# Performance work log

Measured on AMD Instinct MI355X. Metric: run time of the kernel, lower is better.

## Reference

```python
import jax, jax.numpy as jnp
import numpy as np

L, H, P, R = 4096, 1024, 512, 16
DT_MIN, DT_MAX = 1e-3, 1e-1

def setup_inputs() -> dict:
    key = jax.random.key(0)
    ks = jax.random.split(key, 16)
    return {
        "input_sequence": jax.random.normal(ks[0], (L, H), jnp.float32),
        # HiPPO-like eigenvalues: negative real part, spread imaginary part
        "Lambda_re": (-0.5 * jax.random.uniform(ks[1], (P,), jnp.float32) - 1e-2),
        "Lambda_im": 3.0 * jax.random.normal(ks[2], (P,), jnp.float32),
        "B_re": jax.random.normal(ks[3], (P, H), jnp.float32) / np.float32(np.sqrt(H)),
        "B_im": jax.random.normal(ks[4], (P, H), jnp.float32) / np.float32(np.sqrt(H)),
        "C_re": jax.random.normal(ks[5], (H, 2 * P), jnp.float32) / np.float32(np.sqrt(2 * P)),
        "C_im": jax.random.normal(ks[6], (H, 2 * P), jnp.float32) / np.float32(np.sqrt(2 * P)),
        "E_re": 0.01 * jax.random.normal(ks[7], (P, R), jnp.float32),
        "E_im": 0.01 * jax.random.normal(ks[8], (P, R), jnp.float32),
        "F_re": 0.01 * jax.random.normal(ks[9], (R, P), jnp.float32),
        "F_im": 0.01 * jax.random.normal(ks[10], (R, P), jnp.float32),
        "D": jax.random.normal(ks[11], (H,), jnp.float32),
        "log_step": np.float32(np.log(DT_MIN)) + jax.random.uniform(ks[12], (P,), jnp.float32) * np.float32(np.log(DT_MAX) - np.log(DT_MIN)),
        "Delta_t_diag": 0.01 * jax.random.normal(ks[13], (L, R), jnp.float32),
    }

def _scan_op(q_i, q_j):
    # diagonal linear recurrence combine: x_j = A_j * x_i + b_j
    A_i, b_i = q_i
    A_j, b_j = q_j
    return (A_j * A_i, A_j * b_i + b_j)

def reference(input_sequence, Lambda_re, Lambda_im, B_re, B_im, C_re, C_im,
              E_re, E_im, F_re, F_im, D, log_step, Delta_t_diag):
    # clip_eigs=True: enforce left-half-plane
    Lam = jnp.clip(Lambda_re, None, -1e-4) + 1j * Lambda_im            # (P,)
    step = jnp.exp(log_step)                                           # (P,)  step_rescale=1.0
    # zoh discretization
    Lambda_bar = jnp.exp(Lam * step)                                   # (P,)
    B_tilde = B_re + 1j * B_im                                         # (P,H)
    B_bar = ((Lambda_bar - 1.0) / Lam)[:, None] * B_tilde              # (P,H)
    # Lambda extension: diag(E @ diag(d_l) @ F)[p] = sum_r E[p,r] d_l[r] F[r,p]
    E = E_re + 1j * E_im                                               # (P,R)
    F = F_re + 1j * F_im                                               # (R,P)
    EF = E.T * F                                                       # (R,P)
    ext = Delta_t_diag.astype(EF.dtype) @ EF                           # (L,P)
    Lambda_elements = Lambda_bar[None, :] + ext                        # (L,P)
    Bu_elements = input_sequence.astype(B_bar.dtype) @ B_bar.T         # (L,P)
    _, xs_f = jax.lax.associative_scan(_scan_op, (Lambda_elements, Bu_elements))
    _, xs_b = jax.lax.associative_scan(_scan_op, (Lambda_elements, Bu_elements), reverse=True)
    xs = jnp.concatenate((xs_f, xs_b), axis=-1)                        # (L,2P) bidirectional
    C_tilde = C_re + 1j * C_im                                         # (H,2P)
    ys = 2.0 * (xs @ C_tilde.T).real                                   # conj_sym=True -> 2*Re
    return ys + D * input_sequence                                     # feedthrough
```

## Files before the change

### kernel.cpp

```cpp
#include <hip/hip_runtime.h>

#define LL 4096
#define HH 1024
#define PP 512
#define RR 16
#define CH 128
#define CL 32

typedef _Float16 f16x8 __attribute__((ext_vector_type(8)));
typedef float f32x4 __attribute__((ext_vector_type(4)));
typedef unsigned short u16;
typedef unsigned int u32;

#define MF16(a, b, c) __builtin_amdgcn_mfma_f32_16x16x32_f16(a, b, c, 0, 0, 0)

__device__ __forceinline__ u16 h16(float x) {
  _Float16 h = (_Float16)x;
  return __builtin_bit_cast(u16, h);
}
__device__ __forceinline__ float f16f(u16 v) {
  return (float)__builtin_bit_cast(_Float16, v);
}

__global__ void precompute_kernel(const float* __restrict__ Lre, const float* __restrict__ Lim,
                                  const float* __restrict__ lst,
                                  const float* __restrict__ Ere, const float* __restrict__ Eim,
                                  const float* __restrict__ Fre, const float* __restrict__ Fim,
                                  float* __restrict__ Lbr, float* __restrict__ Lbi,
                                  float* __restrict__ cfr, float* __restrict__ cfi,
                                  float* __restrict__ EFr, float* __restrict__ EFi)
{
  int p = blockIdx.x * blockDim.x + threadIdx.x;
  if (p >= PP) return;
  float lre = fminf(Lre[p], -1e-4f);
  float lim = Lim[p];
  float st  = expf(lst[p]);
  float er  = expf(lre * st);
  float s, c;
  sincosf(lim * st, &s, &c);
  float lbr = er * c, lbi = er * s;
  Lbr[p] = lbr; Lbi[p] = lbi;
  float den = lre * lre + lim * lim;
  float nr  = lbr - 1.0f;
  cfr[p] = (nr * lre + lbi * lim) / den;
  cfi[p] = (lbi * lre - nr * lim) / den;
  for (int r = 0; r < RR; ++r) {
    float e_r = Ere[p * RR + r], e_i = Eim[p * RR + r];
    float f_r = Fre[r * PP + p], f_i = Fim[r * PP + p];
    EFr[r * PP + p] = e_r * f_r - e_i * f_i;
    EFi[r * PP + p] = e_r * f_i + e_i * f_r;
  }
}

__global__ __launch_bounds__(256) void prep2_kernel(
    const float* __restrict__ Bre, const float* __restrict__ Bim,
    const float* __restrict__ cfr, const float* __restrict__ cfi,
    const float* __restrict__ Cre, const float* __restrict__ Cim,
    const float* __restrict__ Dt, const float* __restrict__ EFr,
    const float* __restrict__ EFi,
    u16* __restrict__ B1, u32* __restrict__ B2, u32* __restrict__ LE)
{
  int g = blockIdx.x, t = threadIdx.x;
  if (g < 512) {
    int base = (g * 256 + t) * 4;
    int p = base >> 10, col = base & 1023;
    float cr = cfr[p], ci = cfi[p];
    float4 br = *(const float4*)&Bre[base];
    float4 bi = *(const float4*)&Bim[base];
    ushort4 rp, ip;
    rp.x = h16(cr*br.x - ci*bi.x); ip.x = h16(cr*bi.x + ci*br.x);
    rp.y = h16(cr*br.y - ci*bi.y); ip.y = h16(cr*bi.y + ci*br.y);
    rp.z = h16(cr*br.z - ci*bi.z); ip.z = h16(cr*bi.z + ci*br.z);
    rp.w = h16(cr*br.w - ci*bi.w); ip.w = h16(cr*bi.w + ci*br.w);
    *(ushort4*)&B1[(size_t)(2 * p) * 1024 + col] = rp;
    *(ushort4*)&B1[(size_t)(2 * p + 1) * 1024 + col] = ip;
  } else if (g < 1536) {
    int base = ((g - 512) * 256 + t) * 4;
    float4 a = *(const float4*)&Cre[base];
    float4 b = *(const float4*)&Cim[base];
    uint4 o;
    o.x = (u32)h16(a.x) | ((u32)h16(-b.x) << 16);
    o.y = (u32)h16(a.y) | ((u32)h16(-b.y) << 16);
    o.z = (u32)h16(a.z) | ((u32)h16(-b.z) << 16);
    o.w = (u32)h16(a.w) | ((u32)h16(-b.w) << 16);
    *(uint4*)&B2[base] = o;
  } else {
    int gid = (g - 1536) * 256 + t;
    int l  = gid >> 7;
    int pq = (gid & 127) << 2;
    float4 ar = {0.f, 0.f, 0.f, 0.f};
    float4 ai = {0.f, 0.f, 0.f, 0.f};
#pragma unroll
    for (int r = 0; r < RR; ++r) {
      float d = Dt[l * RR + r];
      float4 er = *(const float4*)&EFr[r * PP + pq];
      float4 ei = *(const float4*)&EFi[r * PP + pq];
      ar.x = fmaf(d, er.x, ar.x); ar.y = fmaf(d, er.y, ar.y);
      ar.z = fmaf(d, er.z, ar.z); ar.w = fmaf(d, er.w, ar.w);
      ai.x = fmaf(d, ei.x, ai.x); ai.y = fmaf(d, ei.y, ai.y);
      ai.z = fmaf(d, ei.z, ai.z); ai.w = fmaf(d, ei.w, ai.w);
    }
    uint4 o;
    o.x = (u32)h16(ar.x) | ((u32)h16(ai.x) << 16);
    o.y = (u32)h16(ar.y) | ((u32)h16(ai.y) << 16);
    o.z = (u32)h16(ar.z) | ((u32)h16(ai.z) << 16);
    o.w = (u32)h16(ar.w) | ((u32)h16(ai.w) << 16);
    *(uint4*)&LE[(size_t)l * PP + pq] = o;
  }
}

template<int EPI, bool ACVT>
__global__ __launch_bounds__(256) void gemm_k(
    const void* __restrict__ Asrc, const u16* __restrict__ Bsrc, int Kp,
    void* __restrict__ outv, const float* __restrict__ Dv,
    const float* __restrict__ Uep)
{
  __shared__ __align__(16) uint4 lds[2 * 16 * 64];
  int bid = blockIdx.x;
  int n0 = (bid & 7) * 128;
  int m0 = (bid >> 3) * 128;
  int t = threadIdx.x, lane = t & 63, w = t >> 6;
  int wr = w >> 1, wc = w & 1;
  int rl = lane & 15, kg = lane >> 4;
  int srow = t >> 1, shalf = t & 1;
  int NT = Kp / 32;

  const float* Af = (const float*)Asrc;
  const u16*   Ah = (const u16*)Asrc;

  f32x4 acc[4][4];
#pragma unroll
  for (int m = 0; m < 4; ++m)
#pragma unroll
    for (int n = 0; n < 4; ++n) acc[m][n] = (f32x4){0.f, 0.f, 0.f, 0.f};

  struct Frags { uint4 a[2]; uint4 b[2]; };
  auto LOAD = [&](int kt) -> Frags {
    Frags f;
    if constexpr (ACVT) {
      const float* p = Af + (size_t)(m0 + srow) * Kp + kt * 32 + shalf * 16;
#pragma unroll
      for (int j = 0; j < 2; ++j) {
        float4 a = *(const float4*)(p + j * 8), b = *(const float4*)(p + j * 8 + 4);
        f16x8 r;
        r[0] = (_Float16)a.x; r[1] = (_Float16)a.y; r[2] = (_Float16)a.z; r[3] = (_Float16)a.w;
        r[4] = (_Float16)b.x; r[5] = (_Float16)b.y; r[6] = (_Float16)b.z; r[7] = (_Float16)b.w;
        f.a[j] = __builtin_bit_cast(uint4, r);
      }
    } else {
      const u16* p = Ah + (size_t)(m0 + srow) * Kp + kt * 32 + shalf * 16;
      f.a[0] = *(const uint4*)p;
      f.a[1] = *(const uint4*)(p + 8);
    }
    const u16* q = Bsrc + (size_t)(n0 + srow) * Kp + kt * 32 + shalf * 16;
    f.b[0] = *(const uint4*)q;
    f.b[1] = *(const uint4*)(q + 8);
    return f;
  };
  auto WRITE = [&](int buf, const Frags& f) {
#pragma unroll
    for (int j = 0; j < 2; ++j) {
      int kq = shalf * 2 + j;
      int slot = kq * 16 + ((srow & 15) ^ (2 * kq));
      int seg = srow >> 4;
      lds[buf * 1024 + seg * 64 + slot] = f.a[j];
      lds[buf * 1024 + (8 + seg) * 64 + slot] = f.b[j];
    }
  };

  Frags nxt, far;
  WRITE(0, LOAD(0));
  nxt = LOAD(1);
  __syncthreads();

  for (int kt = 0; kt < NT; ++kt) {
    int c = kt & 1;
    if (kt + 2 < NT) far = LOAD(kt + 2);
    int rslot = kg * 16 + (rl ^ (kg * 2));
    f16x8 af[4], bf[4];
#pragma unroll
    for (int m = 0; m < 4; ++m)
      af[m] = __builtin_bit_cast(f16x8, lds[c * 1024 + (wr * 4 + m) * 64 + rslot]);
#pragma unroll
    for (int n = 0; n < 4; ++n)
      bf[n] = __builtin_bit_cast(f16x8, lds[c * 1024 + (8 + wc * 4 + n) * 64 + rslot]);
#pragma unroll
    for (int m = 0; m < 4; ++m)
#pragma unroll
      for (int n = 0; n < 4; ++n)
        acc[m][n] = MF16(af[m], bf[n], acc[m][n]);
    if (kt + 1 < NT) WRITE(c ^ 1, nxt);
    nxt = far;
    __syncthreads();
  }

  if constexpr (EPI == 1) {
    float* Y = (float*)outv;
#pragma unroll
    for (int n = 0; n < 4; ++n) {
      int col = n0 + wc * 64 + n * 16 + rl;
      float dv = Dv[col];
#pragma unroll
      for (int m = 0; m < 4; ++m)
#pragma unroll
        for (int j = 0; j < 4; ++j) {
          int row = m0 + wr * 64 + m * 16 + kg * 4 + j;
          size_t idx = (size_t)row * 1024 + col;
          Y[idx] = 2.f * acc[m][n][j] + dv * Uep[idx];
        }
    }
  } else {
    u32* P2 = (u32*)outv;
#pragma unroll
    for (int n = 0; n < 4; ++n) {
      int col = n0 + wc * 64 + n * 16 + rl;
#pragma unroll
      for (int m = 0; m < 4; ++m)
#pragma unroll
        for (int j = 0; j < 4; ++j) {
          int row = m0 + wr * 64 + m * 16 + kg * 4 + j;
          u32 hx = (u32)h16(acc[m][n][j]);
          u32 px = (u32)__shfl_xor((int)hx, 1);
          if ((rl & 1) == 0)
            P2[(size_t)row * 512 + (col >> 1)] = hx | (px << 16);
        }
    }
  }
}

__global__ __launch_bounds__(256) void scan_agg_kernel(
    const float* __restrict__ Lbr, const float* __restrict__ Lbi,
    const u32* __restrict__ LE, const u32* __restrict__ P2,
    float* __restrict__ aggAr, float* __restrict__ aggAi,
    float* __restrict__ aggBr, float* __restrict__ aggBi)
{
  int tid = blockIdx.x * 256 + threadIdx.x;
  int p   = tid & (PP - 1);
  int c   = (tid >> 9) & (CH - 1);
  int dir = tid >> 16;
  float lbr = Lbr[p], lbi = Lbi[p];
  float Ar = 1.f, Ai = 0.f, br = 0.f, bi = 0.f;
  int base = c * CL;
#pragma unroll
  for (int g = 0; g < CL / 8; ++g) {
    float ar8[8], ai8[8], br8[8], bi8[8];
#pragma unroll
    for (int u = 0; u < 8; ++u) {
      int l = base + g * 8 + u;
      int phys = dir ? (LL - 1 - l) : l;
      u32 v = LE[(size_t)phys * PP + p];
      u32 bv = P2[(size_t)phys * PP + p];
      ar8[u] = lbr + f16f((u16)(v & 0xffff));
      ai8[u] = lbi + f16f((u16)(v >> 16));
      br8[u] = f16f((u16)(bv & 0xffff));
      bi8[u] = f16f((u16)(bv >> 16));
    }
#pragma unroll
    for (int u = 0; u < 8; ++u) {
      float nAr = ar8[u] * Ar - ai8[u] * Ai;
      float nAi = ar8[u] * Ai + ai8[u] * Ar;
      float nbr = fmaf(ar8[u], br, fmaf(-ai8[u], bi, br8[u]));
      float nbi = fmaf(ar8[u], bi, fmaf( ai8[u], br, bi8[u]));
      Ar = nAr; Ai = nAi; br = nbr; bi = nbi;
    }
  }
  aggAr[tid] = Ar; aggAi[tid] = Ai; aggBr[tid] = br; aggBi[tid] = bi;
}

__global__ __launch_bounds__(256) void scan_carry_kernel(
    const float* __restrict__ aggAr, const float* __restrict__ aggAi,
    const float* __restrict__ aggBr, const float* __restrict__ aggBi,
    float* __restrict__ carR, float* __restrict__ carI)
{
  int tid = blockIdx.x * 256 + threadIdx.x;
  int p   = tid & (PP - 1);
  int dir = tid >> 9;
  float xr = 0.f, xi = 0.f;
  for (int c = 0; c < CH; ++c) {
    int idx = (dir * CH + c) * PP + p;
    carR[idx] = xr; carI[idx] = xi;
    float ar = aggAr[idx], ai = aggAi[idx];
    float br = aggBr[idx], bi = aggBi[idx];
    float nr = fmaf(ar, xr, fmaf(-ai, xi, br));
    float ni = fmaf(ar, xi, fmaf( ai, xr, bi));
    xr = nr; xi = ni;
  }
}

__global__ __launch_bounds__(256) void scan_apply_kernel(
    const float* __restrict__ Lbr, const float* __restrict__ Lbi,
    const u32* __restrict__ LE, const u32* __restrict__ P2,
    const float* __restrict__ carR, const float* __restrict__ carI,
    u32* __restrict__ A2)
{
  int tid = blockIdx.x * 256 + threadIdx.x;
  int p   = tid & (PP - 1);
  int c   = (tid >> 9) & (CH - 1);
  int dir = tid >> 16;
  float lbr = Lbr[p], lbi = Lbi[p];
  float xr = carR[tid], xi = carI[tid];
  int base = c * CL;
  int cofs = dir * PP + p;
#pragma unroll
  for (int g = 0; g < CL / 8; ++g) {
    float ar8[8], ai8[8], br8[8], bi8[8];
#pragma unroll
    for (int u = 0; u < 8; ++u) {
      int l = base + g * 8 + u;
      int phys = dir ? (LL - 1 - l) : l;
      u32 v = LE[(size_t)phys * PP + p];
      u32 bv = P2[(size_t)phys * PP + p];
      ar8[u] = lbr + f16f((u16)(v & 0xffff));
      ai8[u] = lbi + f16f((u16)(v >> 16));
      br8[u] = f16f((u16)(bv & 0xffff));
      bi8[u] = f16f((u16)(bv >> 16));
    }
#pragma unroll
    for (int u = 0; u < 8; ++u) {
      float nr = fmaf(ar8[u], xr, fmaf(-ai8[u], xi, br8[u]));
      float ni = fmaf(ar8[u], xi, fmaf( ai8[u], xr, bi8[u]));
      xr = nr; xi = ni;
      int l = base + g * 8 + u;
      int phys = dir ? (LL - 1 - l) : l;
      A2[(size_t)phys * 1024 + cofs] = (u32)h16(xr) | ((u32)h16(xi) << 16);
    }
  }
}

extern "C" void kernel_launch(void* const* d_in, const int* in_sizes, int n_in,
                              void* d_out, int out_size, void* d_ws, size_t ws_size,
                              hipStream_t stream)
{
  const float* U   = (const float*)d_in[0];
  const float* Lre = (const float*)d_in[1];
  const float* Lim = (const float*)d_in[2];
  const float* Bre = (const float*)d_in[3];
  const float* Bim = (const float*)d_in[4];
  const float* Cre = (const float*)d_in[5];
  const float* Cim = (const float*)d_in[6];
  const float* Ere = (const float*)d_in[7];
  const float* Eim = (const float*)d_in[8];
  const float* Fre = (const float*)d_in[9];
  const float* Fim = (const float*)d_in[10];
  const float* Dv  = (const float*)d_in[11];
  const float* lst = (const float*)d_in[12];
  const float* Dt  = (const float*)d_in[13];
  float* Y = (float*)d_out;

  char* wsb = (char*)d_ws;
  size_t o = 0;
  auto alloc = [&](size_t bytes) -> char* {
    char* r = wsb + o; o += (bytes + 255) & ~(size_t)255; return r;
  };
  float* Lbr = (float*)alloc(PP * 4);
  float* Lbi = (float*)alloc(PP * 4);
  float* cfr = (float*)alloc(PP * 4);
  float* cfi = (float*)alloc(PP * 4);
  float* EFr = (float*)alloc((size_t)RR * PP * 4);
  float* EFi = (float*)alloc((size_t)RR * PP * 4);
  u16* B1 = (u16*)alloc((size_t)1024 * 1024 * 2);
  u32* B2 = (u32*)alloc((size_t)1024 * 1024 * 4);
  u32* LE = (u32*)alloc((size_t)LL * PP * 4);
  u32* P2 = (u32*)alloc((size_t)LL * PP * 4);
  u32* A2 = (u32*)alloc((size_t)LL * 1024 * 4);
  const int NAGG = 2 * CH * PP;
  float* aggAr = (float*)alloc((size_t)NAGG * 4);
  float* aggAi = (float*)alloc((size_t)NAGG * 4);
  float* aggBr = (float*)alloc((size_t)NAGG * 4);
  float* aggBi = (float*)alloc((size_t)NAGG * 4);
  float* carR  = (float*)alloc((size_t)NAGG * 4);
  float* carI  = (float*)alloc((size_t)NAGG * 4);

  precompute_kernel<<<2, 256, 0, stream>>>(Lre, Lim, lst, Ere, Eim, Fre, Fim,
                                           Lbr, Lbi, cfr, cfi, EFr, EFi);
  prep2_kernel<<<3584, 256, 0, stream>>>(Bre, Bim, cfr, cfi, Cre, Cim,
                                         Dt, EFr, EFi, B1, B2, LE);
  gemm_k<2, true><<<256, 256, 0, stream>>>(U, B1, 1024, P2, nullptr, nullptr);
  scan_agg_kernel<<<2 * CH * PP / 256, 256, 0, stream>>>(Lbr, Lbi, LE, P2,
                                                         aggAr, aggAi, aggBr, aggBi);
  scan_carry_kernel<<<4, 256, 0, stream>>>(aggAr, aggAi, aggBr, aggBi, carR, carI);
  scan_apply_kernel<<<2 * CH * PP / 256, 256, 0, stream>>>(Lbr, Lbi, LE, P2, carR, carI, A2);
  gemm_k<1, false><<<256, 256, 0, stream>>>(A2, (const u16*)B2, 2048, Y, Dv, U);
}
```

Baseline: 127.7 us.

## Use 8 waves per GEMM block with 64-wide K tiles

The GEMM kernel now runs 512 threads (8 waves) per 128x128 tile instead of 256. Each wave computes a 64x32 sub-tile, and the K step per iteration doubles to 64 with a larger LDS double buffer. The goal is more latency hiding per CU and half as many barriers per K. The cost is a doubled LDS footprint, less register reuse per wave (more LDS reads per MFMA), and only 256 blocks across the CUs.

```diff
diff --git a/kernel.cpp b/kernel.cpp
--- a/kernel.cpp
+++ b/kernel.cpp
@@ -110,35 +110,35 @@
 }
 
 template<int EPI, bool ACVT>
-__global__ __launch_bounds__(256) void gemm_k(
+__global__ __launch_bounds__(512) void gemm_k8(
     const void* __restrict__ Asrc, const u16* __restrict__ Bsrc, int Kp,
     void* __restrict__ outv, const float* __restrict__ Dv,
     const float* __restrict__ Uep)
 {
-  __shared__ __align__(16) uint4 lds[2 * 16 * 64];
+  __shared__ __align__(16) uint4 lds[2 * 32 * 64];
+  int NT = Kp / 64;
   int bid = blockIdx.x;
   int n0 = (bid & 7) * 128;
   int m0 = (bid >> 3) * 128;
   int t = threadIdx.x, lane = t & 63, w = t >> 6;
-  int wr = w >> 1, wc = w & 1;
+  int wr = w >> 2, wc = w & 3;
   int rl = lane & 15, kg = lane >> 4;
-  int srow = t >> 1, shalf = t & 1;
-  int NT = Kp / 32;
+  int srow = t >> 2, cch = t & 3;
 
   const float* Af = (const float*)Asrc;
   const u16*   Ah = (const u16*)Asrc;
 
-  f32x4 acc[4][4];
+  f32x4 acc[4][2];
 #pragma unroll
   for (int m = 0; m < 4; ++m)
 #pragma unroll
-    for (int n = 0; n < 4; ++n) acc[m][n] = (f32x4){0.f, 0.f, 0.f, 0.f};
+    for (int n = 0; n < 2; ++n) acc[m][n] = (f32x4){0.f, 0.f, 0.f, 0.f};
 
   struct Frags { uint4 a[2]; uint4 b[2]; };
   auto LOAD = [&](int kt) -> Frags {
     Frags f;
     if constexpr (ACVT) {
-      const float* p = Af + (size_t)(m0 + srow) * Kp + kt * 32 + shalf * 16;
+      const float* p = Af + (size_t)(m0 + srow) * Kp + kt * 64 + cch * 16;
 #pragma unroll
       for (int j = 0; j < 2; ++j) {
         float4 a = *(const float4*)(p + j * 8), b = *(const float4*)(p + j * 8 + 4);
@@ -148,11 +148,11 @@
         f.a[j] = __builtin_bit_cast(uint4, r);
       }
     } else {
-      const u16* p = Ah + (size_t)(m0 + srow) * Kp + kt * 32 + shalf * 16;
+      const u16* p = Ah + (size_t)(m0 + srow) * Kp + kt * 64 + cch * 16;
       f.a[0] = *(const uint4*)p;
       f.a[1] = *(const uint4*)(p + 8);
     }
-    const u16* q = Bsrc + (size_t)(n0 + srow) * Kp + kt * 32 + shalf * 16;
+    const u16* q = Bsrc + (size_t)(n0 + srow) * Kp + kt * 64 + cch * 16;
     f.b[0] = *(const uint4*)q;
     f.b[1] = *(const uint4*)(q + 8);
     return f;
@@ -160,11 +160,12 @@
   auto WRITE = [&](int buf, const Frags& f) {
 #pragma unroll
     for (int j = 0; j < 2; ++j) {
-      int kq = shalf * 2 + j;
-      int slot = kq * 16 + ((srow & 15) ^ (2 * kq));
-      int seg = srow >> 4;
-      lds[buf * 1024 + seg * 64 + slot] = f.a[j];
-      lds[buf * 1024 + (8 + seg) * 64 + slot] = f.b[j];
+      int kq = cch * 2 + j;
+      int c = kq & 3;
+      int slot = c * 16 + ((srow & 15) ^ (c * 2));
+      int seg = (srow >> 4) * 2 + (kq >> 2);
+      lds[buf * 2048 + seg * 64 + slot] = f.a[j];
+      lds[buf * 2048 + (16 + seg) * 64 + slot] = f.b[j];
     }
   };
 
@@ -177,18 +178,26 @@
     int c = kt & 1;
     if (kt + 2 < NT) far = LOAD(kt + 2);
     int rslot = kg * 16 + (rl ^ (kg * 2));
-    f16x8 af[4], bf[4];
+    f16x8 af[4][2], bf[2][2];
 #pragma unroll
     for (int m = 0; m < 4; ++m)
-      af[m] = __builtin_bit_cast(f16x8, lds[c * 1024 + (wr * 4 + m) * 64 + rslot]);
-#pragma unroll
-    for (int n = 0; n < 4; ++n)
-      bf[n] = __builtin_bit_cast(f16x8, lds[c * 1024 + (8 + wc * 4 + n) * 64 + rslot]);
-#pragma unroll
-    for (int m = 0; m < 4; ++m)
-#pragma unroll
-      for (int n = 0; n < 4; ++n)
-        acc[m][n] = MF16(af[m], bf[n], acc[m][n]);
+#pragma unroll
+      for (int ks = 0; ks < 2; ++ks)
+        af[m][ks] = __builtin_bit_cast(f16x8,
+            lds[c * 2048 + ((wr * 4 + m) * 2 + ks) * 64 + rslot]);
+#pragma unroll
+    for (int n = 0; n < 2; ++n)
+#pragma unroll
+      for (int ks = 0; ks < 2; ++ks)
+        bf[n][ks] = __builtin_bit_cast(f16x8,
+            lds[c * 2048 + (16 + (wc * 2 + n) * 2 + ks) * 64 + rslot]);
+#pragma unroll
+    for (int ks = 0; ks < 2; ++ks)
+#pragma unroll
+      for (int m = 0; m < 4; ++m)
+#pragma unroll
+        for (int n = 0; n < 2; ++n)
+          acc[m][n] = MF16(af[m][ks], bf[n][ks], acc[m][n]);
     if (kt + 1 < NT) WRITE(c ^ 1, nxt);
     nxt = far;
     __syncthreads();
@@ -197,8 +206,8 @@
   if constexpr (EPI == 1) {
     float* Y = (float*)outv;
 #pragma unroll
-    for (int n = 0; n < 4; ++n) {
-      int col = n0 + wc * 64 + n * 16 + rl;
+    for (int n = 0; n < 2; ++n) {
+      int col = n0 + wc * 32 + n * 16 + rl;
       float dv = Dv[col];
 #pragma unroll
       for (int m = 0; m < 4; ++m)
@@ -212,8 +221,8 @@
   } else {
     u32* P2 = (u32*)outv;
 #pragma unroll
-    for (int n = 0; n < 4; ++n) {
-      int col = n0 + wc * 64 + n * 16 + rl;
+    for (int n = 0; n < 2; ++n) {
+      int col = n0 + wc * 32 + n * 16 + rl;
 #pragma unroll
       for (int m = 0; m < 4; ++m)
 #pragma unroll
@@ -375,10 +384,10 @@
                                            Lbr, Lbi, cfr, cfi, EFr, EFi);
   prep2_kernel<<<3584, 256, 0, stream>>>(Bre, Bim, cfr, cfi, Cre, Cim,
                                          Dt, EFr, EFi, B1, B2, LE);
-  gemm_k<2, true><<<256, 256, 0, stream>>>(U, B1, 1024, P2, nullptr, nullptr);
+  gemm_k8<2, true><<<256, 512, 0, stream>>>(U, B1, 1024, P2, nullptr, nullptr);
   scan_agg_kernel<<<2 * CH * PP / 256, 256, 0, stream>>>(Lbr, Lbi, LE, P2,
                                                          aggAr, aggAi, aggBr, aggBi);
   scan_carry_kernel<<<4, 256, 0, stream>>>(aggAr, aggAi, aggBr, aggBi, carR, carI);
   scan_apply_kernel<<<2 * CH * PP / 256, 256, 0, stream>>>(Lbr, Lbi, LE, P2, carR, carI, A2);
-  gemm_k<1, false><<<256, 256, 0, stream>>>(A2, (const u16*)B2, 2048, Y, Dv, U);
-}
+  gemm_k8<1, false><<<256, 512, 0, stream>>>(A2, (const u16*)B2, 2048, Y, Dv, U);
+}
```

Result: faster. 111.9 us (-12.3%).
